# Performance work log

Measured on AMD Instinct MI355X. Metric: run time of the kernel, lower is better.

Reference implementation:

```python
import jax, jax.numpy as jnp
import numpy as np

DIM = 256
N_TAPES = 4
HEAD_DIM = 64  # mem_size
HT = HEAD_DIM * N_TAPES  # 256
QKVA = 3 * HT + 11 * N_TAPES  # 812
EPS = 1e-12


def _normalize(x, axis):
    n = jnp.sqrt(jnp.sum(x * x, axis=axis, keepdims=True))
    return x / jnp.maximum(n, EPS)


def setup_inputs() -> dict:
    key = jax.random.key(0)
    ks = jax.random.split(key, 8)
    L_tgt, L_src, B = 128, 64, 512
    s = 1.0 / np.sqrt(DIM)
    return {
        "tgt": jax.random.normal(ks[0], (L_tgt, B, DIM), jnp.float32),
        "src": jax.random.normal(ks[1], (L_src, B, DIM), jnp.float32),
        "W_ih": jax.random.uniform(ks[2], (4 * DIM, DIM), jnp.float32, -s, s),
        "W_hh": jax.random.uniform(ks[3], (4 * DIM, DIM), jnp.float32, -s, s),
        "b_ih": jax.random.uniform(ks[4], (4 * DIM,), jnp.float32, -s, s),
        "b_hh": jax.random.uniform(ks[5], (4 * DIM,), jnp.float32, -s, s),
        "Wqkva_w": jax.random.uniform(ks[6], (QKVA, DIM), jnp.float32, -s, s),
        "Wqkva_b": jax.random.uniform(ks[7], (QKVA,), jnp.float32, -s, s),
    }


def _step(carry, x, W_ih, W_hh, b_ih, b_hh, Wqkva_w, Wqkva_b):
    tape, rpos, wpos, h, c = carry  # tape: [L,B,T,C], rpos/wpos: [L,B,T]
    B = x.shape[0]
    # LSTMCell (torch gate order: i, f, g, o)
    gates = x @ W_ih.T + b_ih + h @ W_hh.T + b_hh
    i, f, g, o = jnp.split(gates, 4, axis=-1)
    c = jax.nn.sigmoid(f) * c + jax.nn.sigmoid(i) * jnp.tanh(g)
    h = jax.nn.sigmoid(o) * jnp.tanh(c)
    qkva = h @ Wqkva_w.T + Wqkva_b  # [B, 812]
    query = _normalize(qkva[:, :HT].reshape(B, N_TAPES, HEAD_DIM), axis=-1)
    # note: `key` slice in the original is empty and unused
    value = qkva[:, 2 * HT:3 * HT].reshape(B, N_TAPES, HEAD_DIM)
    action = qkva[:, 3 * HT:].reshape(B, N_TAPES, 11)
    read_dir = jax.nn.softmax(action[:, :, :4], axis=-1)
    write_dir = jax.nn.softmax(action[:, :, 4:8], axis=-1)
    rwe = jax.nn.sigmoid(action[:, :, 8:])
    oldval = jnp.einsum('lbtc,lbt->btc', tape, wpos)
    newmem = jnp.einsum('lbt,btc->lbtc', wpos,
                        value * rwe[:, :, 1:2] - oldval * rwe[:, :, 2:3])
    ntape = tape + newmem
    rval = jnp.einsum('lbtc,lbt->btc', tape, rpos * rwe[:, :, 0]).reshape(B, -1)
    jpos = _normalize(jnp.einsum('lbtc,btc->lbt', tape, query), axis=0)
    next_w = jnp.roll(wpos, 1, axis=0)
    prev_w = jnp.roll(wpos, -1, axis=0)
    nwpos = (prev_w * write_dir[None, :, :, 0] + wpos * write_dir[None, :, :, 1]
             + next_w * write_dir[None, :, :, 2] + jpos * write_dir[None, :, :, 3])
    next_r = jnp.roll(rpos, 1, axis=0)
    prev_r = jnp.roll(rpos, -1, axis=0)
    nrpos = (prev_r * read_dir[None, :, :, 0] + rpos * read_dir[None, :, :, 1]
             + next_r * read_dir[None, :, :, 2] + jpos * read_dir[None, :, :, 3])
    return (ntape, nrpos, nwpos, h, c), rval


def reference(tgt, src, W_ih, W_hh, b_ih, b_hh, Wqkva_w, Wqkva_b):
    L_src, B = src.shape[0], src.shape[1]
    tape = src.reshape(L_src, B, N_TAPES, HEAD_DIM)
    pos0 = jnp.zeros((L_src, B, N_TAPES), src.dtype).at[0].set(1.0)
    h = jnp.zeros((B, DIM), src.dtype)
    c = jnp.zeros((B, DIM), src.dtype)

    def step(carry, x):
        return _step(carry, x, W_ih, W_hh, b_ih, b_hh, Wqkva_w, Wqkva_b)

    _, read_outs = jax.lax.scan(step, (tape, pos0, pos0, h, c), tgt)
    return read_outs  # [seqlen, B, dim]
```

## Files before the change

kernel.cpp:

```cpp
#include <hip/hip_runtime.h>
#include <hip/hip_bf16.h>

typedef short short8_v __attribute__((ext_vector_type(8)));
typedef float f32x4 __attribute__((ext_vector_type(4)));

#define QC 576

__device__ __forceinline__ size_t swz_e(int r, int k, int KC) {
  return ((size_t)((r >> 4) * KC + (k >> 5)) * 64 + (r & 15) + (((k >> 3) & 3) << 4)) * 8 + (k & 7);
}

__device__ __forceinline__ float wave_sum(float v) {
#pragma unroll
  for (int off = 32; off > 0; off >>= 1) v += __shfl_xor(v, off);
  return v;
}

__device__ __forceinline__ float sigf(float x) { return 1.f / (1.f + __expf(-x)); }
__device__ __forceinline__ float tfast(float x) {
  float e = __expf(2.f * x);
  return 1.f - 2.f / (e + 1.f);
}

template <typename T>
__device__ __forceinline__ T ald(const T* p) {
  return __hip_atomic_load(p, __ATOMIC_RELAXED, __HIP_MEMORY_SCOPE_AGENT);
}
template <typename T>
__device__ __forceinline__ void ast(T* p, T v) {
  __hip_atomic_store(p, v, __ATOMIC_RELAXED, __HIP_MEMORY_SCOPE_AGENT);
}


__global__ void prep_weights(const float* __restrict__ W_ih, const float* __restrict__ W_hh,
                             __hip_bfloat16* __restrict__ Wcat) {
  int idx = blockIdx.x * blockDim.x + threadIdx.x;
  if (idx >= 1024 * 512) return;
  int jj = idx >> 9, k = idx & 511;
  int chunk = jj >> 6, gate = (jj >> 4) & 3, r = jj & 15;
  int j = gate * 256 + chunk * 16 + r;
  float v = (k < 256) ? W_ih[j * 256 + k] : W_hh[j * 256 + (k - 256)];
  Wcat[swz_e(jj, k, 16)] = __float2bfloat16(v);
}

__global__ void prep_wq(const float* __restrict__ Wq_w, const float* __restrict__ Wq_b,
                        __hip_bfloat16* __restrict__ Wq, float* __restrict__ biasq) {
  int idx = blockIdx.x * blockDim.x + threadIdx.x;
  if (idx >= 576 * 256) return;
  int n = idx >> 8, k = idx & 255;
  int orig = (n < 256) ? n : (n < 556 ? n + 256 : -1);
  float v = (orig >= 0) ? Wq_w[orig * 256 + k] : 0.f;
  Wq[swz_e(n, k, 8)] = __float2bfloat16(v);
  if (k == 0) biasq[n] = (orig >= 0) ? Wq_b[orig] : 0.f;
}

__global__ void prep_tgt(const float* __restrict__ tgt, __hip_bfloat16* __restrict__ tswz) {
  for (size_t idx = (size_t)blockIdx.x * blockDim.x + threadIdx.x; idx < (size_t)128 * 131072;
       idx += (size_t)gridDim.x * blockDim.x) {
    int t = (int)(idx >> 17);
    int rem = (int)(idx & 131071);
    int b = rem >> 8, k = rem & 255;
    tswz[(size_t)t * 131072 + swz_e(b, k, 8)] = __float2bfloat16(tgt[idx]);
  }
}

__global__ void reset_bars(unsigned* __restrict__ bars) {
  int i = blockIdx.x * blockDim.x + threadIdx.x;
  if (i < 2048) bars[i] = 0u;
}

#define DYN_LDS 79872

__global__ __launch_bounds__(256, 2) void persist(
    const short8_v* __restrict__ tswz, const short8_v* __restrict__ Wcat,
    const short8_v* __restrict__ Wq, const float* __restrict__ biasq,
    const float* __restrict__ b_ih, const float* __restrict__ b_hh,
    unsigned short* __restrict__ hG,
    float* __restrict__ qkva,
    float* __restrict__ out, const float* __restrict__ src, unsigned* __restrict__ bars) {
  extern __shared__ float lds[];
  const int tid = threadIdx.x;
  const int w = tid >> 6, lane = tid & 63;
  const int m = blockIdx.x & 31, cgrp = blockIdx.x >> 5;
  unsigned* grpbar = bars + m * 64;

  f32x4* Tc = (f32x4*)lds + (size_t)w * 1024;
  float* WS = lds + 16384 + w * 128;
  float* gbuf = lds + 16896;
  float* QN = lds + 16896 + w * 64;
  unsigned long long* hstage_u64 = (unsigned long long*)(lds + 17920);
  const short8_v* hstage_s8 = (const short8_v*)(lds + 17920);

  const int g = lane >> 4, c4 = lane & 15;

  const int b = 16 * m + cgrp;
  const int tp = w;
#pragma unroll
  for (int i = 0; i < 16; ++i) {
    int row = i * 4 + g;
    f32x4 v = *(const f32x4*)(src + (size_t)row * 131072 + b * 256 + tp * 64 + c4 * 4);
    Tc[row * 16 + (c4 ^ (row & 15))] = v;
  }
  float rp = (lane == 0) ? 1.f : 0.f, wp = rp;
  float wpPrev = 0.f;
  f32x4 dvp4 = {0.f, 0.f, 0.f, 0.f};
  bool bar_ok = true;

  const int erow = tid >> 4, ecol = tid & 15;
  const int jh = 16 * cgrp + ecol;
  const float bI = b_ih[jh] + b_hh[jh];
  const float bF = b_ih[256 + jh] + b_hh[256 + jh];
  const float bG_ = b_ih[512 + jh] + b_hh[512 + jh];
  const float bO = b_ih[768 + jh] + b_hh[768 + jh];
  float c_reg = 0.f;
  const unsigned hIdx32 =
      (unsigned)(((m * 8 + (jh >> 5)) * 64 + erow + 16 * ((jh >> 3) & 3)) * 4 + ((jh >> 1) & 3));

  const int qcnt = (cgrp < 4) ? 3 : 2;
  const int qst = (cgrp < 4) ? 3 * cgrp : 12 + 2 * (cgrp - 4);
  const int qtile = qst + w;

  short8_v bFr[16];
#pragma unroll
  for (int kc = 0; kc < 16; ++kc) bFr[kc] = Wcat[((4 * cgrp + w) * 16 + kc) * 64 + lane];
  short8_v bQ[8];
  float bqv = 0.f;
  int n0 = 0;
  if (w < qcnt) {
    n0 = qtile * 16 + (lane & 15);
    bqv = biasq[n0];
#pragma unroll
    for (int kc = 0; kc < 8; ++kc) bQ[kc] = Wq[(qtile * 8 + kc) * 64 + lane];
  }

#pragma unroll 1
  for (int p = 0; p <= 129; ++p) {
    const int hrd = (p + 1) & 1, hwr = p & 1;
    const int s = p - 2;

    float a_[11];
    f32x4 q4, val4;
    if (s >= 0) {
      const float* qrow = qkva + (size_t)(s & 1) * (512 * QC) + (size_t)b * QC;
#pragma unroll
      for (int j = 0; j < 11; ++j) a_[j] = ald(qrow + 512 + tp * 11 + j);
      unsigned long long u0 = ald((const unsigned long long*)(qrow + tp * 64 + c4 * 4));
      unsigned long long u1 = ald((const unsigned long long*)(qrow + tp * 64 + c4 * 4 + 2));
      unsigned long long v0 = ald((const unsigned long long*)(qrow + 256 + tp * 64 + c4 * 4));
      unsigned long long v1 = ald((const unsigned long long*)(qrow + 256 + tp * 64 + c4 * 4 + 2));
      float2 qa = __builtin_bit_cast(float2, u0), qb = __builtin_bit_cast(float2, u1);
      float2 va = __builtin_bit_cast(float2, v0), vb = __builtin_bit_cast(float2, v1);
      q4 = (f32x4){qa.x, qa.y, qb.x, qb.y};
      val4 = (f32x4){va.x, va.y, vb.x, vb.y};
    }
    short8_v aF[8];
    if (p < 128) {
      const short8_v* xg = tswz + (size_t)p * 16384;
#pragma unroll
      for (int kc = 0; kc < 8; ++kc) aF[kc] = xg[(m * 8 + kc) * 64 + lane];
    }
    if (p >= 1 && p <= 128) {
      const unsigned long long* hsrc =
          (const unsigned long long*)(hG + (size_t)hrd * 131072) + (size_t)m * 1024;
#pragma unroll
      for (int j = 0; j < 4; ++j) {
        unsigned long long v = ald(hsrc + tid + 256 * j);
        hstage_u64[tid + 256 * j] = v;
      }
    }
    __syncthreads();
    if (p < 128) {
      f32x4 acc = {0.f, 0.f, 0.f, 0.f};
#pragma unroll
      for (int kc = 0; kc < 8; ++kc)
        acc = __builtin_amdgcn_mfma_f32_16x16x32_bf16(aF[kc], bFr[kc], acc, 0, 0, 0);
      if (p > 0) {
#pragma unroll
        for (int kc = 8; kc < 16; ++kc) {
          short8_v a = hstage_s8[(kc - 8) * 64 + lane];
          acc = __builtin_amdgcn_mfma_f32_16x16x32_bf16(a, bFr[kc], acc, 0, 0, 0);
        }
      }
#pragma unroll
      for (int r = 0; r < 4; ++r)
        gbuf[(w * 16 + ((lane >> 4) * 4 + r)) * 16 + (lane & 15)] = acc[r];
    }
    __syncthreads();
    if (p < 128) {
      float gi = gbuf[(0 * 16 + erow) * 16 + ecol] + bI;
      float gf = gbuf[(1 * 16 + erow) * 16 + ecol] + bF;
      float gg = gbuf[(2 * 16 + erow) * 16 + ecol] + bG_;
      float go = gbuf[(3 * 16 + erow) * 16 + ecol] + bO;
      float cc = sigf(gf) * c_reg + sigf(gi) * tfast(gg);
      c_reg = cc;
      float hh = sigf(go) * tfast(cc);
      __hip_bfloat16 hb16 = __float2bfloat16(hh);
      unsigned own = (unsigned)(*(unsigned short*)&hb16);
      unsigned other = (unsigned)__shfl_xor((int)own, 1) & 0xFFFFu;
      if ((ecol & 1) == 0) {
        unsigned pack = (other << 16) | own;
        ast((unsigned*)(hG + (size_t)hwr * 131072) + hIdx32, pack);
      }
    }
    if (p >= 1 && p <= 128 && w < qcnt) {
      f32x4 qa = {0.f, 0.f, 0.f, 0.f};
#pragma unroll
      for (int kc = 0; kc < 8; ++kc)
        qa = __builtin_amdgcn_mfma_f32_16x16x32_bf16(hstage_s8[kc * 64 + lane], bQ[kc], qa, 0, 0, 0);
      float* qw = qkva + (size_t)((p - 1) & 1) * (512 * QC);
#pragma unroll
      for (int r = 0; r < 4; ++r)
        ast(&qw[(size_t)(16 * m + (lane >> 4) * 4 + r) * QC + n0], qa[r] + bqv);
    }
    asm volatile("s_waitcnt vmcnt(0)" ::: "memory");
    __syncthreads();
    if (tid == 0 && p < 129)
      __hip_atomic_fetch_add(grpbar, 1u, __ATOMIC_RELAXED, __HIP_MEMORY_SCOPE_AGENT);
    if (s >= 0) {
      float m1 = fmaxf(fmaxf(a_[0], a_[1]), fmaxf(a_[2], a_[3]));
      float e0 = __expf(a_[0] - m1), e1 = __expf(a_[1] - m1), e2 = __expf(a_[2] - m1),
            e3 = __expf(a_[3] - m1);
      float inv = 1.f / (e0 + e1 + e2 + e3);
      float rd0 = e0 * inv, rd1 = e1 * inv, rd2 = e2 * inv, rd3 = e3 * inv;
      float m2 = fmaxf(fmaxf(a_[4], a_[5]), fmaxf(a_[6], a_[7]));
      float f0 = __expf(a_[4] - m2), f1 = __expf(a_[5] - m2), f2 = __expf(a_[6] - m2),
            f3 = __expf(a_[7] - m2);
      float inv2 = 1.f / (f0 + f1 + f2 + f3);
      float wd0 = f0 * inv2, wd1 = f1 * inv2, wd2 = f2 * inv2, wd3 = f3 * inv2;
      float rwe0 = sigf(a_[8]), rwe1 = sigf(a_[9]), rwe2 = sigf(a_[10]);
      float ss = q4[0] * q4[0] + q4[1] * q4[1] + q4[2] * q4[2] + q4[3] * q4[3];
#pragma unroll
      for (int off = 1; off < 16; off <<= 1) ss += __shfl_xor(ss, off);
      float qninv = 1.f / fmaxf(sqrtf(ss), 1e-12f);
      f32x4 qn4 = q4 * qninv;
      *(float2*)&WS[lane * 2] = make_float2(wp, rp * rwe0);
      if (g == 0) *(f32x4*)&QN[c4 * 4] = qn4;
      f32x4 oa = {0.f, 0.f, 0.f, 0.f}, ra = oa;
#pragma unroll
      for (int i = 0; i < 16; ++i) {
        int row = i * 4 + g;
        float wO = __shfl(wpPrev, row);
        float2 wrN = *(const float2*)&WS[row * 2];
        int ti = row * 16 + (c4 ^ (row & 15));
        f32x4 v = Tc[ti];
        v += wO * dvp4;
        Tc[ti] = v;
        oa += wrN.x * v;
        ra += wrN.y * v;
      }
#pragma unroll
      for (int off = 16; off <= 32; off <<= 1) {
        f32x4 t;
        t[0] = __shfl_xor(oa[0], off); t[1] = __shfl_xor(oa[1], off);
        t[2] = __shfl_xor(oa[2], off); t[3] = __shfl_xor(oa[3], off);
        oa += t;
        t[0] = __shfl_xor(ra[0], off); t[1] = __shfl_xor(ra[1], off);
        t[2] = __shfl_xor(ra[2], off); t[3] = __shfl_xor(ra[3], off);
        ra += t;
      }
      dvp4 = val4 * rwe1 - oa * rwe2;
      if (g == 0)
        *(f32x4*)(out + (size_t)s * 131072 + b * 256 + tp * 64 + c4 * 4) = ra;
      float jq = 0.f;
#pragma unroll
      for (int j = 0; j < 16; ++j) {
        f32x4 v = Tc[lane * 16 + (j ^ (lane & 15))];
        f32x4 qv = *(const f32x4*)&QN[j * 4];
        jq += v[0] * qv[0] + v[1] * qv[1] + v[2] * qv[2] + v[3] * qv[3];
      }
      float jsum = wave_sum(jq * jq);
      float jp = jq / fmaxf(sqrtf(jsum), 1e-12f);
      float next_w = __shfl(wp, (lane + 63) & 63);
      float prev_w = __shfl(wp, (lane + 1) & 63);
      float next_r = __shfl(rp, (lane + 63) & 63);
      float prev_r = __shfl(rp, (lane + 1) & 63);
      wpPrev = wp;
      wp = prev_w * wd0 + wp * wd1 + next_w * wd2 + jp * wd3;
      rp = prev_r * rd0 + rp * rd1 + next_r * rd2 + jp * rd3;
    }
    if (p < 129) {
      __syncthreads();
      if (tid == 0) {
        unsigned target = 16u * (unsigned)(p + 1);
        if (bar_ok) {
          long long t0 = (long long)__builtin_amdgcn_s_memrealtime();
          while (ald(grpbar) < target) {
            __builtin_amdgcn_s_sleep(8);
            if ((long long)__builtin_amdgcn_s_memrealtime() - t0 > 100000000LL) {
              bar_ok = false;
              break;
            }
          }
        }
        asm volatile("" ::: "memory");
      }
      __syncthreads();
    }
  }
}


extern "C" void kernel_launch(void* const* d_in, const int* in_sizes, int n_in, void* d_out,
                              int out_size, void* d_ws, size_t ws_size, hipStream_t stream) {
  const float* tgt = (const float*)d_in[0];
  const float* src = (const float*)d_in[1];
  const float* W_ih = (const float*)d_in[2];
  const float* W_hh = (const float*)d_in[3];
  const float* b_ih = (const float*)d_in[4];
  const float* b_hh = (const float*)d_in[5];
  const float* Wq_w = (const float*)d_in[6];
  const float* Wq_b = (const float*)d_in[7];
  float* out = (float*)d_out;

  char* ws = (char*)d_ws;
  size_t off = 0;
  auto alloc = [&](size_t bytes) -> void* {
    void* p = ws + off;
    off = (off + bytes + 255) & ~(size_t)255;
    return p;
  };
  unsigned* bars = (unsigned*)alloc(2048 * 4);
  float* qkva = (float*)alloc((size_t)2 * 512 * QC * 4);
  unsigned short* hG = (unsigned short*)alloc((size_t)2 * 131072 * 2);
  __hip_bfloat16* Wcat = (__hip_bfloat16*)alloc((size_t)1024 * 512 * 2);
  __hip_bfloat16* Wq = (__hip_bfloat16*)alloc((size_t)576 * 256 * 2);
  float* biasq = (float*)alloc((size_t)576 * 4);
  __hip_bfloat16* tswz = (__hip_bfloat16*)alloc((size_t)128 * 131072 * 2);

  reset_bars<<<8, 256, 0, stream>>>(bars);
  prep_weights<<<2048, 256, 0, stream>>>(W_ih, W_hh, Wcat);
  prep_wq<<<576, 256, 0, stream>>>(Wq_w, Wq_b, Wq, biasq);
  prep_tgt<<<8192, 256, 0, stream>>>(tgt, tswz);

  hipFuncSetAttribute((const void*)persist, hipFuncAttributeMaxDynamicSharedMemorySize, DYN_LDS);

  persist<<<dim3(512), dim3(256), DYN_LDS, stream>>>(
      (const short8_v*)tswz, (const short8_v*)Wcat, (const short8_v*)Wq, biasq, b_ih, b_hh, hG,
      qkva, out, src, bars);
}
```

Measured before the change: 1.002 ms.

## Specialize waves into tape and LSTM roles in 512-thread persistent blocks

Halves the grid to 256 blocks of 512 threads. Waves 0-3 each handle two tape heads, so a block covers two batch rows. Waves 4-7 compute two LSTM gate tiles and extra qkva tiles, loading h straight from global into registers instead of staging it in LDS, and reading weights from global each step rather than keeping them in registers. An intra-block LDS counter lets the LSTM waves signal the group barrier without waiting for the tape waves, so tape work can overlap the matmul/arrive path. The cost is double LDS per block, more global weight traffic per step, and serialized per-wave work across two tapes.

```diff
diff --git a/kernel.cpp b/kernel.cpp
--- a/kernel.cpp
+++ b/kernel.cpp
@@ -3,6 +3,7 @@
 
 typedef short short8_v __attribute__((ext_vector_type(8)));
 typedef float f32x4 __attribute__((ext_vector_type(4)));
+typedef unsigned long long u64x2_v __attribute__((ext_vector_type(2)));
 
 #define QC 576
 
@@ -69,9 +70,9 @@
   if (i < 2048) bars[i] = 0u;
 }
 
-#define DYN_LDS 79872
-
-__global__ __launch_bounds__(256, 2) void persist(
+#define DYN_LDS 145664
+
+__global__ __launch_bounds__(512, 2) void persist(
     const short8_v* __restrict__ tswz, const short8_v* __restrict__ Wcat,
     const short8_v* __restrict__ Wq, const float* __restrict__ biasq,
     const float* __restrict__ b_ih, const float* __restrict__ b_hh,
@@ -81,207 +82,277 @@
   extern __shared__ float lds[];
   const int tid = threadIdx.x;
   const int w = tid >> 6, lane = tid & 63;
-  const int m = blockIdx.x & 31, cgrp = blockIdx.x >> 5;
+  const int m = (int)blockIdx.x & 31, cgrp = (int)blockIdx.x >> 5;
   unsigned* grpbar = bars + m * 64;
-
-  f32x4* Tc = (f32x4*)lds + (size_t)w * 1024;
-  float* WS = lds + 16384 + w * 128;
-  float* gbuf = lds + 16896;
-  float* QN = lds + 16896 + w * 64;
-  unsigned long long* hstage_u64 = (unsigned long long*)(lds + 17920);
-  const short8_v* hstage_s8 = (const short8_v*)(lds + 17920);
+  unsigned* gctr = (unsigned*)(lds + 36352);
+  float* gbuf = lds + 34304;
 
   const int g = lane >> 4, c4 = lane & 15;
-
-  const int b = 16 * m + cgrp;
-  const int tp = w;
-#pragma unroll
-  for (int i = 0; i < 16; ++i) {
-    int row = i * 4 + g;
-    f32x4 v = *(const f32x4*)(src + (size_t)row * 131072 + b * 256 + tp * 64 + c4 * 4);
-    Tc[row * 16 + (c4 ^ (row & 15))] = v;
+  const bool isTape = (w < 4);
+  const int gw = w & 3;
+
+  if (tid == 0) *gctr = 0u;
+  bool bar_ok = true;
+
+  float wp[2], rp[2], wpPrev[2];
+  f32x4 dvp4[2];
+  int bq[2], tpq[2];
+  if (isTape) {
+#pragma unroll
+    for (int u = 0; u < 2; ++u) {
+      int q = 2 * w + u;
+      bq[u] = 16 * m + 2 * cgrp + (q >> 2);
+      tpq[u] = q & 3;
+      f32x4* Tc = (f32x4*)lds + (size_t)q * 1024;
+#pragma unroll
+      for (int i = 0; i < 16; ++i) {
+        int row = i * 4 + g;
+        f32x4 v = *(const f32x4*)(src + (size_t)row * 131072 + bq[u] * 256 + tpq[u] * 64 + c4 * 4);
+        Tc[row * 16 + (c4 ^ (row & 15))] = v;
+      }
+      wp[u] = (lane == 0) ? 1.f : 0.f;
+      rp[u] = wp[u];
+      wpPrev[u] = 0.f;
+      dvp4[u] = (f32x4){0.f, 0.f, 0.f, 0.f};
+    }
   }
-  float rp = (lane == 0) ? 1.f : 0.f, wp = rp;
-  float wpPrev = 0.f;
-  f32x4 dvp4 = {0.f, 0.f, 0.f, 0.f};
-  bool bar_ok = true;
-
-  const int erow = tid >> 4, ecol = tid & 15;
-  const int jh = 16 * cgrp + ecol;
-  const float bI = b_ih[jh] + b_hh[jh];
-  const float bF = b_ih[256 + jh] + b_hh[256 + jh];
-  const float bG_ = b_ih[512 + jh] + b_hh[512 + jh];
-  const float bO = b_ih[768 + jh] + b_hh[768 + jh];
-  float c_reg = 0.f;
-  const unsigned hIdx32 =
-      (unsigned)(((m * 8 + (jh >> 5)) * 64 + erow + 16 * ((jh >> 3) & 3)) * 4 + ((jh >> 1) & 3));
-
-  const int qcnt = (cgrp < 4) ? 3 : 2;
-  const int qst = (cgrp < 4) ? 3 * cgrp : 12 + 2 * (cgrp - 4);
-  const int qtile = qst + w;
-
-  short8_v bFr[16];
-#pragma unroll
-  for (int kc = 0; kc < 16; ++kc) bFr[kc] = Wcat[((4 * cgrp + w) * 16 + kc) * 64 + lane];
-  short8_v bQ[8];
-  float bqv = 0.f;
-  int n0 = 0;
-  if (w < qcnt) {
-    n0 = qtile * 16 + (lane & 15);
-    bqv = biasq[n0];
-#pragma unroll
-    for (int kc = 0; kc < 8; ++kc) bQ[kc] = Wq[(qtile * 8 + kc) * 64 + lane];
+
+  const int erow = (tid & 255) >> 4, ecol = tid & 15;
+  float c_reg[2] = {0.f, 0.f};
+  float bIa[2], bFa[2], bGa[2], bOa[2];
+  unsigned hIdx32[2];
+  int qtile[2] = {0, 0}, nqt = 0, n0[2] = {0, 0};
+  float bqv[2] = {0.f, 0.f};
+  if (!isTape) {
+#pragma unroll
+    for (int u = 0; u < 2; ++u) {
+      int jh = 32 * cgrp + 16 * u + ecol;
+      bIa[u] = b_ih[jh] + b_hh[jh];
+      bFa[u] = b_ih[256 + jh] + b_hh[256 + jh];
+      bGa[u] = b_ih[512 + jh] + b_hh[512 + jh];
+      bOa[u] = b_ih[768 + jh] + b_hh[768 + jh];
+      hIdx32[u] =
+          (unsigned)(((m * 8 + (jh >> 5)) * 64 + erow + 16 * ((jh >> 3) & 3)) * 4 + ((jh >> 1) & 3));
+    }
+    const int qcnt = (cgrp < 4) ? 5 : 4;
+    const int qst = (cgrp < 4) ? 5 * cgrp : 20 + 4 * (cgrp - 4);
+    qtile[0] = qst + gw;
+    nqt = 1;
+    if (gw == 0 && qcnt == 5) {
+      qtile[1] = qst + 4;
+      nqt = 2;
+    }
+#pragma unroll
+    for (int u = 0; u < 2; ++u) {
+      int qt = (u < nqt) ? qtile[u] : qtile[0];
+      n0[u] = qt * 16 + (lane & 15);
+      bqv[u] = biasq[n0[u]];
+    }
   }
+  __syncthreads();
 
 #pragma unroll 1
   for (int p = 0; p <= 129; ++p) {
     const int hrd = (p + 1) & 1, hwr = p & 1;
     const int s = p - 2;
 
-    float a_[11];
-    f32x4 q4, val4;
-    if (s >= 0) {
-      const float* qrow = qkva + (size_t)(s & 1) * (512 * QC) + (size_t)b * QC;
-#pragma unroll
-      for (int j = 0; j < 11; ++j) a_[j] = ald(qrow + 512 + tp * 11 + j);
-      unsigned long long u0 = ald((const unsigned long long*)(qrow + tp * 64 + c4 * 4));
-      unsigned long long u1 = ald((const unsigned long long*)(qrow + tp * 64 + c4 * 4 + 2));
-      unsigned long long v0 = ald((const unsigned long long*)(qrow + 256 + tp * 64 + c4 * 4));
-      unsigned long long v1 = ald((const unsigned long long*)(qrow + 256 + tp * 64 + c4 * 4 + 2));
-      float2 qa = __builtin_bit_cast(float2, u0), qb = __builtin_bit_cast(float2, u1);
-      float2 va = __builtin_bit_cast(float2, v0), vb = __builtin_bit_cast(float2, v1);
-      q4 = (f32x4){qa.x, qa.y, qb.x, qb.y};
-      val4 = (f32x4){va.x, va.y, vb.x, vb.y};
-    }
-    short8_v aF[8];
-    if (p < 128) {
-      const short8_v* xg = tswz + (size_t)p * 16384;
-#pragma unroll
-      for (int kc = 0; kc < 8; ++kc) aF[kc] = xg[(m * 8 + kc) * 64 + lane];
-    }
-    if (p >= 1 && p <= 128) {
-      const unsigned long long* hsrc =
-          (const unsigned long long*)(hG + (size_t)hrd * 131072) + (size_t)m * 1024;
-#pragma unroll
-      for (int j = 0; j < 4; ++j) {
-        unsigned long long v = ald(hsrc + tid + 256 * j);
-        hstage_u64[tid + 256 * j] = v;
+    float a_[2][11];
+    f32x4 q4[2], val4[2];
+    short8_v aF[8], aH[8];
+    float rd[2][4], wd[2][4];
+    if (isTape) {
+      if (s >= 0) {
+#pragma unroll
+        for (int u = 0; u < 2; ++u) {
+          const float* qrow = qkva + (size_t)(s & 1) * (512 * QC) + (size_t)bq[u] * QC;
+#pragma unroll
+          for (int j = 0; j < 11; ++j) a_[u][j] = ald(qrow + 512 + tpq[u] * 11 + j);
+          unsigned long long u0 = ald((const unsigned long long*)(qrow + tpq[u] * 64 + c4 * 4));
+          unsigned long long u1 = ald((const unsigned long long*)(qrow + tpq[u] * 64 + c4 * 4 + 2));
+          unsigned long long v0 = ald((const unsigned long long*)(qrow + 256 + tpq[u] * 64 + c4 * 4));
+          unsigned long long v1 =
+              ald((const unsigned long long*)(qrow + 256 + tpq[u] * 64 + c4 * 4 + 2));
+          float2 qa = __builtin_bit_cast(float2, u0), qb = __builtin_bit_cast(float2, u1);
+          float2 va = __builtin_bit_cast(float2, v0), vb = __builtin_bit_cast(float2, v1);
+          q4[u] = (f32x4){qa.x, qa.y, qb.x, qb.y};
+          val4[u] = (f32x4){va.x, va.y, vb.x, vb.y};
+        }
+      }
+    } else {
+      if (p < 128) {
+        const short8_v* xg = tswz + (size_t)p * 16384;
+#pragma unroll
+        for (int kc = 0; kc < 8; ++kc) aF[kc] = xg[(m * 8 + kc) * 64 + lane];
+      }
+      if (p >= 1 && p <= 128) {
+        const unsigned long long* hsrc = (const unsigned long long*)(hG + (size_t)hrd * 131072);
+#pragma unroll
+        for (int kc = 0; kc < 8; ++kc) {
+          size_t bi = ((size_t)(m * 8 + kc) * 64 + lane) * 2;
+          u64x2_v t2;
+          t2.x = ald(hsrc + bi);
+          t2.y = ald(hsrc + bi + 1);
+          aH[kc] = __builtin_bit_cast(short8_v, t2);
+        }
+      }
+    }
+
+    if (isTape) {
+      if (s >= 0) {
+#pragma unroll
+        for (int u = 0; u < 2; ++u) {
+          float m1 = fmaxf(fmaxf(a_[u][0], a_[u][1]), fmaxf(a_[u][2], a_[u][3]));
+          float e0 = __expf(a_[u][0] - m1), e1 = __expf(a_[u][1] - m1), e2 = __expf(a_[u][2] - m1),
+                e3 = __expf(a_[u][3] - m1);
+          float inv = 1.f / (e0 + e1 + e2 + e3);
+          rd[u][0] = e0 * inv; rd[u][1] = e1 * inv; rd[u][2] = e2 * inv; rd[u][3] = e3 * inv;
+          float m2 = fmaxf(fmaxf(a_[u][4], a_[u][5]), fmaxf(a_[u][6], a_[u][7]));
+          float f0 = __expf(a_[u][4] - m2), f1 = __expf(a_[u][5] - m2), f2 = __expf(a_[u][6] - m2),
+                f3 = __expf(a_[u][7] - m2);
+          float inv2 = 1.f / (f0 + f1 + f2 + f3);
+          wd[u][0] = f0 * inv2; wd[u][1] = f1 * inv2; wd[u][2] = f2 * inv2; wd[u][3] = f3 * inv2;
+          float rwe0 = sigf(a_[u][8]), rwe1 = sigf(a_[u][9]), rwe2 = sigf(a_[u][10]);
+          float ss = q4[u][0] * q4[u][0] + q4[u][1] * q4[u][1] + q4[u][2] * q4[u][2] +
+                     q4[u][3] * q4[u][3];
+#pragma unroll
+          for (int off = 1; off < 16; off <<= 1) ss += __shfl_xor(ss, off);
+          float qninv = 1.f / fmaxf(sqrtf(ss), 1e-12f);
+          f32x4 qn4 = q4[u] * qninv;
+          const int q = 2 * w + u;
+          float* WSq = lds + 32768 + q * 128;
+          float* QNq = lds + 33792 + q * 64;
+          *(float2*)&WSq[lane * 2] = make_float2(wp[u], rp[u] * rwe0);
+          if (g == 0) *(f32x4*)&QNq[c4 * 4] = qn4;
+          f32x4* Tc = (f32x4*)lds + (size_t)q * 1024;
+          f32x4 oa = {0.f, 0.f, 0.f, 0.f}, ra = oa;
+#pragma unroll
+          for (int i = 0; i < 16; ++i) {
+            int row = i * 4 + g;
+            float wO = __shfl(wpPrev[u], row);
+            float2 wrN = *(const float2*)&WSq[row * 2];
+            int ti = row * 16 + (c4 ^ (row & 15));
+            f32x4 v = Tc[ti];
+            v += wO * dvp4[u];
+            Tc[ti] = v;
+            oa += wrN.x * v;
+            ra += wrN.y * v;
+          }
+#pragma unroll
+          for (int off = 16; off <= 32; off <<= 1) {
+            f32x4 t;
+            t[0] = __shfl_xor(oa[0], off); t[1] = __shfl_xor(oa[1], off);
+            t[2] = __shfl_xor(oa[2], off); t[3] = __shfl_xor(oa[3], off);
+            oa += t;
+            t[0] = __shfl_xor(ra[0], off); t[1] = __shfl_xor(ra[1], off);
+            t[2] = __shfl_xor(ra[2], off); t[3] = __shfl_xor(ra[3], off);
+            ra += t;
+          }
+          dvp4[u] = val4[u] * rwe1 - oa * rwe2;
+          if (g == 0)
+            *(f32x4*)(out + (size_t)s * 131072 + bq[u] * 256 + tpq[u] * 64 + c4 * 4) = ra;
+        }
+      }
+    } else {
+      if (p < 128) {
+#pragma unroll
+        for (int t = 0; t < 2; ++t) {
+          const int T = 8 * cgrp + 4 * t + gw;
+          f32x4 acc = {0.f, 0.f, 0.f, 0.f};
+#pragma unroll
+          for (int kc = 0; kc < 8; ++kc)
+            acc = __builtin_amdgcn_mfma_f32_16x16x32_bf16(aF[kc], Wcat[(T * 16 + kc) * 64 + lane],
+                                                          acc, 0, 0, 0);
+          if (p > 0) {
+#pragma unroll
+            for (int kc = 8; kc < 16; ++kc)
+              acc = __builtin_amdgcn_mfma_f32_16x16x32_bf16(
+                  aH[kc - 8], Wcat[(T * 16 + kc) * 64 + lane], acc, 0, 0, 0);
+          }
+#pragma unroll
+          for (int r = 0; r < 4; ++r)
+            gbuf[((t * 4 + gw) * 16 + ((lane >> 4) * 4 + r)) * 16 + (lane & 15)] = acc[r];
+        }
       }
     }
     __syncthreads();
-    if (p < 128) {
-      f32x4 acc = {0.f, 0.f, 0.f, 0.f};
-#pragma unroll
-      for (int kc = 0; kc < 8; ++kc)
-        acc = __builtin_amdgcn_mfma_f32_16x16x32_bf16(aF[kc], bFr[kc], acc, 0, 0, 0);
-      if (p > 0) {
-#pragma unroll
-        for (int kc = 8; kc < 16; ++kc) {
-          short8_v a = hstage_s8[(kc - 8) * 64 + lane];
-          acc = __builtin_amdgcn_mfma_f32_16x16x32_bf16(a, bFr[kc], acc, 0, 0, 0);
-        }
-      }
-#pragma unroll
-      for (int r = 0; r < 4; ++r)
-        gbuf[(w * 16 + ((lane >> 4) * 4 + r)) * 16 + (lane & 15)] = acc[r];
+
+    if (isTape) {
+      if (s >= 0) {
+#pragma unroll
+        for (int u = 0; u < 2; ++u) {
+          const int q = 2 * w + u;
+          f32x4* Tc = (f32x4*)lds + (size_t)q * 1024;
+          float* QNq = lds + 33792 + q * 64;
+          float jq = 0.f;
+#pragma unroll
+          for (int j = 0; j < 16; ++j) {
+            f32x4 v = Tc[lane * 16 + (j ^ (lane & 15))];
+            f32x4 qv = *(const f32x4*)&QNq[j * 4];
+            jq += v[0] * qv[0] + v[1] * qv[1] + v[2] * qv[2] + v[3] * qv[3];
+          }
+          float jsum = wave_sum(jq * jq);
+          float jp = jq / fmaxf(sqrtf(jsum), 1e-12f);
+          float next_w = __shfl(wp[u], (lane + 63) & 63);
+          float prev_w = __shfl(wp[u], (lane + 1) & 63);
+          float next_r = __shfl(rp[u], (lane + 63) & 63);
+          float prev_r = __shfl(rp[u], (lane + 1) & 63);
+          wpPrev[u] = wp[u];
+          wp[u] = prev_w * wd[u][0] + wp[u] * wd[u][1] + next_w * wd[u][2] + jp * wd[u][3];
+          rp[u] = prev_r * rd[u][0] + rp[u] * rd[u][1] + next_r * rd[u][2] + jp * rd[u][3];
+        }
+      }
+    } else {
+      if (p < 128) {
+#pragma unroll
+        for (int u = 0; u < 2; ++u) {
+          float gi = gbuf[((u * 4 + 0) * 16 + erow) * 16 + ecol] + bIa[u];
+          float gf = gbuf[((u * 4 + 1) * 16 + erow) * 16 + ecol] + bFa[u];
+          float gg = gbuf[((u * 4 + 2) * 16 + erow) * 16 + ecol] + bGa[u];
+          float go = gbuf[((u * 4 + 3) * 16 + erow) * 16 + ecol] + bOa[u];
+          float cc = sigf(gf) * c_reg[u] + sigf(gi) * tfast(gg);
+          c_reg[u] = cc;
+          float hh = sigf(go) * tfast(cc);
+          __hip_bfloat16 hb16 = __float2bfloat16(hh);
+          unsigned own = (unsigned)(*(unsigned short*)&hb16);
+          unsigned other = (unsigned)__shfl_xor((int)own, 1) & 0xFFFFu;
+          if ((ecol & 1) == 0) {
+            unsigned pack = (other << 16) | own;
+            ast((unsigned*)(hG + (size_t)hwr * 131072) + hIdx32[u], pack);
+          }
+        }
+      }
+      if (p >= 1 && p <= 128) {
+        float* qw = qkva + (size_t)((p - 1) & 1) * (512 * QC);
+#pragma unroll
+        for (int u = 0; u < 2; ++u) {
+          if (u < nqt) {
+            f32x4 qa = {0.f, 0.f, 0.f, 0.f};
+#pragma unroll
+            for (int kc = 0; kc < 8; ++kc)
+              qa = __builtin_amdgcn_mfma_f32_16x16x32_bf16(
+                  aH[kc], Wq[(qtile[u] * 8 + kc) * 64 + lane], qa, 0, 0, 0);
+#pragma unroll
+            for (int r = 0; r < 4; ++r)
+              ast(&qw[(size_t)(16 * m + (lane >> 4) * 4 + r) * QC + n0[u]], qa[r] + bqv[u]);
+          }
+        }
+      }
+      asm volatile("s_waitcnt vmcnt(0)" ::: "memory");
+      if (p < 129) {
+        if (lane == 0)
+          __hip_atomic_fetch_add(gctr, 1u, __ATOMIC_RELAXED, __HIP_MEMORY_SCOPE_WORKGROUP);
+        if (tid == 256) {
+          unsigned tgt4 = 4u * (unsigned)(p + 1);
+          while (__hip_atomic_load(gctr, __ATOMIC_RELAXED, __HIP_MEMORY_SCOPE_WORKGROUP) < tgt4)
+            __builtin_amdgcn_s_sleep(1);
+          __hip_atomic_fetch_add(grpbar, 1u, __ATOMIC_RELAXED, __HIP_MEMORY_SCOPE_AGENT);
+        }
+      }
     }
     __syncthreads();
-    if (p < 128) {
-      float gi = gbuf[(0 * 16 + erow) * 16 + ecol] + bI;
-      float gf = gbuf[(1 * 16 + erow) * 16 + ecol] + bF;
-      float gg = gbuf[(2 * 16 + erow) * 16 + ecol] + bG_;
-      float go = gbuf[(3 * 16 + erow) * 16 + ecol] + bO;
-      float cc = sigf(gf) * c_reg + sigf(gi) * tfast(gg);
-      c_reg = cc;
-      float hh = sigf(go) * tfast(cc);
-      __hip_bfloat16 hb16 = __float2bfloat16(hh);
-      unsigned own = (unsigned)(*(unsigned short*)&hb16);
-      unsigned other = (unsigned)__shfl_xor((int)own, 1) & 0xFFFFu;
-      if ((ecol & 1) == 0) {
-        unsigned pack = (other << 16) | own;
-        ast((unsigned*)(hG + (size_t)hwr * 131072) + hIdx32, pack);
-      }
-    }
-    if (p >= 1 && p <= 128 && w < qcnt) {
-      f32x4 qa = {0.f, 0.f, 0.f, 0.f};
-#pragma unroll
-      for (int kc = 0; kc < 8; ++kc)
-        qa = __builtin_amdgcn_mfma_f32_16x16x32_bf16(hstage_s8[kc * 64 + lane], bQ[kc], qa, 0, 0, 0);
-      float* qw = qkva + (size_t)((p - 1) & 1) * (512 * QC);
-#pragma unroll
-      for (int r = 0; r < 4; ++r)
-        ast(&qw[(size_t)(16 * m + (lane >> 4) * 4 + r) * QC + n0], qa[r] + bqv);
-    }
-    asm volatile("s_waitcnt vmcnt(0)" ::: "memory");
-    __syncthreads();
-    if (tid == 0 && p < 129)
-      __hip_atomic_fetch_add(grpbar, 1u, __ATOMIC_RELAXED, __HIP_MEMORY_SCOPE_AGENT);
-    if (s >= 0) {
-      float m1 = fmaxf(fmaxf(a_[0], a_[1]), fmaxf(a_[2], a_[3]));
-      float e0 = __expf(a_[0] - m1), e1 = __expf(a_[1] - m1), e2 = __expf(a_[2] - m1),
-            e3 = __expf(a_[3] - m1);
-      float inv = 1.f / (e0 + e1 + e2 + e3);
-      float rd0 = e0 * inv, rd1 = e1 * inv, rd2 = e2 * inv, rd3 = e3 * inv;
-      float m2 = fmaxf(fmaxf(a_[4], a_[5]), fmaxf(a_[6], a_[7]));
-      float f0 = __expf(a_[4] - m2), f1 = __expf(a_[5] - m2), f2 = __expf(a_[6] - m2),
-            f3 = __expf(a_[7] - m2);
-      float inv2 = 1.f / (f0 + f1 + f2 + f3);
-      float wd0 = f0 * inv2, wd1 = f1 * inv2, wd2 = f2 * inv2, wd3 = f3 * inv2;
-      float rwe0 = sigf(a_[8]), rwe1 = sigf(a_[9]), rwe2 = sigf(a_[10]);
-      float ss = q4[0] * q4[0] + q4[1] * q4[1] + q4[2] * q4[2] + q4[3] * q4[3];
-#pragma unroll
-      for (int off = 1; off < 16; off <<= 1) ss += __shfl_xor(ss, off);
-      float qninv = 1.f / fmaxf(sqrtf(ss), 1e-12f);
-      f32x4 qn4 = q4 * qninv;
-      *(float2*)&WS[lane * 2] = make_float2(wp, rp * rwe0);
-      if (g == 0) *(f32x4*)&QN[c4 * 4] = qn4;
-      f32x4 oa = {0.f, 0.f, 0.f, 0.f}, ra = oa;
-#pragma unroll
-      for (int i = 0; i < 16; ++i) {
-        int row = i * 4 + g;
-        float wO = __shfl(wpPrev, row);
-        float2 wrN = *(const float2*)&WS[row * 2];
-        int ti = row * 16 + (c4 ^ (row & 15));
-        f32x4 v = Tc[ti];
-        v += wO * dvp4;
-        Tc[ti] = v;
-        oa += wrN.x * v;
-        ra += wrN.y * v;
-      }
-#pragma unroll
-      for (int off = 16; off <= 32; off <<= 1) {
-        f32x4 t;
-        t[0] = __shfl_xor(oa[0], off); t[1] = __shfl_xor(oa[1], off);
-        t[2] = __shfl_xor(oa[2], off); t[3] = __shfl_xor(oa[3], off);
-        oa += t;
-        t[0] = __shfl_xor(ra[0], off); t[1] = __shfl_xor(ra[1], off);
-        t[2] = __shfl_xor(ra[2], off); t[3] = __shfl_xor(ra[3], off);
-        ra += t;
-      }
-      dvp4 = val4 * rwe1 - oa * rwe2;
-      if (g == 0)
-        *(f32x4*)(out + (size_t)s * 131072 + b * 256 + tp * 64 + c4 * 4) = ra;
-      float jq = 0.f;
-#pragma unroll
-      for (int j = 0; j < 16; ++j) {
-        f32x4 v = Tc[lane * 16 + (j ^ (lane & 15))];
-        f32x4 qv = *(const f32x4*)&QN[j * 4];
-        jq += v[0] * qv[0] + v[1] * qv[1] + v[2] * qv[2] + v[3] * qv[3];
-      }
-      float jsum = wave_sum(jq * jq);
-      float jp = jq / fmaxf(sqrtf(jsum), 1e-12f);
-      float next_w = __shfl(wp, (lane + 63) & 63);
-      float prev_w = __shfl(wp, (lane + 1) & 63);
-      float next_r = __shfl(rp, (lane + 63) & 63);
-      float prev_r = __shfl(rp, (lane + 1) & 63);
-      wpPrev = wp;
-      wp = prev_w * wd0 + wp * wd1 + next_w * wd2 + jp * wd3;
-      rp = prev_r * rd0 + rp * rd1 + next_r * rd2 + jp * rd3;
-    }
     if (p < 129) {
-      __syncthreads();
       if (tid == 0) {
-        unsigned target = 16u * (unsigned)(p + 1);
+        unsigned target = 8u * (unsigned)(p + 1);
         if (bar_ok) {
           long long t0 = (long long)__builtin_amdgcn_s_memrealtime();
           while (ald(grpbar) < target) {
@@ -334,7 +405,7 @@
 
   hipFuncSetAttribute((const void*)persist, hipFuncAttributeMaxDynamicSharedMemorySize, DYN_LDS);
 
-  persist<<<dim3(512), dim3(256), DYN_LDS, stream>>>(
+  persist<<<dim3(256), dim3(512), DYN_LDS, stream>>>(
       (const short8_v*)tswz, (const short8_v*)Wcat, (const short8_v*)Wq, biasq, b_ih, b_hh, hG,
       qkva, out, src, bars);
 }
```

Result: slower. 3.363 ms (+235.7%).
